# Performance work log

Hardware: AMD Instinct MI355X
Metric: run time of the kernel (lower is better)

## Reference

```python
import jax, jax.numpy as jnp
import numpy as np

B, H, E, R, T = 2048, 512, 300, 512, 50


def setup_inputs() -> dict:
    key = jax.random.key(0)
    ks = jax.random.split(key, 12)
    s = 0.02  # xavier-ish scale for params
    return {
        "x": jax.random.normal(ks[0], (B, E), jnp.float32),
        "h_enc": jax.random.normal(ks[1], (B, R), jnp.float32),
        "phi_history": jax.random.normal(ks[2], (T, B, H), jnp.float32),
        "cell_history": jax.random.normal(ks[3], (T, B, H), jnp.float32),
        "h_summ": jax.random.normal(ks[4], (B, H), jnp.float32),
        "c_summ": jax.random.normal(ks[5], (B, H), jnp.float32),
        "W_w": jax.random.normal(ks[6], (4 * H, H + E), jnp.float32) * s,
        "W_b": jnp.zeros((4 * H,), jnp.float32),
        "v_w": jax.random.normal(ks[7], (1, H), jnp.float32) * s,
        "v_b": jnp.zeros((1,), jnp.float32),
        "lq_w": jax.random.normal(ks[8], (H, R), jnp.float32) * s,
        "lq_b": jnp.zeros((H,), jnp.float32),
        "lk_w": jax.random.normal(ks[9], (H, H), jnp.float32) * s,
        "lk_b": jnp.zeros((H,), jnp.float32),
        "ls_w": jax.random.normal(ks[10], (H, H), jnp.float32) * s,
        "ls_b": jnp.zeros((H,), jnp.float32),
    }


def reference(x, h_enc, phi_history, cell_history, h_summ, c_summ,
              W_w, W_b, v_w, v_b, lq_w, lq_b, lk_w, lk_b, ls_w, ls_b):
    Hd = h_summ.shape[-1]
    # [T,B,H] -> [B,T,H] (torch.stack(...).transpose(0,1))
    phi = jnp.transpose(phi_history, (1, 0, 2))
    cell = jnp.transpose(cell_history, (1, 0, 2))
    # additive attention over cached history
    q = h_enc @ lq_w.T + lq_b                       # [B,H]
    k = jnp.einsum('bth,ah->bta', phi, lk_w) + lk_b  # [B,T,H]
    su = h_summ @ ls_w.T + ls_b                     # [B,H]
    e = jnp.tanh(q[:, None, :] + k + su[:, None, :])
    scores = jnp.einsum('bth,oh->bto', e, v_w)[..., 0] + v_b[0]  # [B,T]
    p = jax.nn.softmax(scores, axis=-1)
    h_s = jnp.einsum('bt,bth->bh', p, phi)
    c_s = jnp.einsum('bt,bth->bh', p, cell)
    # fused LSTM gates on [h_summ, x]
    gates = jnp.concatenate([h_s, x], axis=1) @ W_w.T + W_b  # [B,4H]
    f_t = jax.nn.sigmoid(gates[:, :Hd])
    o_t = jax.nn.sigmoid(gates[:, Hd:2 * Hd])
    i_t = jax.nn.sigmoid(gates[:, 2 * Hd:3 * Hd])
    ch_t = jnp.tanh(gates[:, 3 * Hd:])
    c_ctrl = f_t * c_s + i_t * ch_t
    h_ctrl = o_t * jnp.tanh(c_ctrl)
    return h_ctrl
```

## Files before the change

### kernel.cpp

```cpp
#include <hip/hip_runtime.h>
#include <math.h>

#define Bm 2048
#define Hm 512
#define Em 300
#define Tm 50
#define KWm 812
#define KWp 832

typedef unsigned short u16;
typedef unsigned int u32;
typedef __attribute__((ext_vector_type(8))) short short8;
typedef __attribute__((ext_vector_type(8))) u16 ushort8v;
typedef __attribute__((ext_vector_type(4))) float f32x4;

__device__ __forceinline__ float sigmoidf_(float x) { return 1.f / (1.f + __expf(-x)); }
__device__ __forceinline__ float tanhfast(float x) { return 1.f - 2.f / (__expf(2.f * x) + 1.f); }

__device__ __forceinline__ u16 bfr(float x) {
    union { float f; u32 u; } c; c.f = x;
    u32 u = c.u;
    u += 0x7FFFu + ((u >> 16) & 1u);
    return (u16)(u >> 16);
}
__device__ __forceinline__ ushort8v cvt8(const float* __restrict__ p) {
    f32x4 v0 = *(const f32x4*)p;
    f32x4 v1 = *(const f32x4*)(p + 4);
    ushort8v r;
    r[0] = bfr(v0[0]); r[1] = bfr(v0[1]); r[2] = bfr(v0[2]); r[3] = bfr(v0[3]);
    r[4] = bfr(v1[0]); r[5] = bfr(v1[1]); r[6] = bfr(v1[2]); r[7] = bfr(v1[3]);
    return r;
}

__device__ __forceinline__ void gload16(const u16* g, u16* l) {
    __builtin_amdgcn_global_load_lds((const __attribute__((address_space(1))) void*)g,
                                     (__attribute__((address_space(3))) void*)l, 16, 0, 0);
}

__global__ __launch_bounds__(256) void k_prep(
        const float* __restrict__ henc, const float* __restrict__ hsum,
        const float* __restrict__ lq, const float* __restrict__ ls,
        const float* __restrict__ Ww, const float* __restrict__ x,
        const float* __restrict__ lkw,
        const float* __restrict__ lqb, const float* __restrict__ lsb,
        const float* __restrict__ lkb, const float* __restrict__ phi,
        u16* __restrict__ Wg, u16* __restrict__ Xb, u16* __restrict__ lkwb,
        float* __restrict__ qbias, u16* __restrict__ phib,
        float* __restrict__ qs) {
    const int job = blockIdx.y;
    const int r = blockIdx.x;
    const int tid = threadIdx.x;
    if (job == 0) {
        for (int c = tid; c < KWp; c += 256)
            Wg[(size_t)r * KWp + c] = (c < KWm) ? bfr(Ww[(size_t)r * KWm + c]) : (u16)0;
    } else if (job == 1) {
        for (int c = 512 + tid; c < KWp; c += 256)
            Xb[(size_t)r * KWp + c] = (c < KWm) ? bfr(x[(size_t)r * Em + (c - 512)]) : (u16)0;
        if (r < 512)
            for (int c = tid; c < 512; c += 256)
                lkwb[(size_t)r * 512 + c] = bfr(lkw[(size_t)r * 512 + c]);
        if (r == 0)
            for (int c = tid; c < 512; c += 256)
                qbias[c] = lqb[c] + lsb[c] + lkb[c];
    } else if (job == 2) {
        const size_t nvec = (size_t)Tm * Bm * 512 / 8;
        for (size_t i = (size_t)r * 256 + tid; i < nvec; i += (size_t)2048 * 256)
            *(ushort8v*)&phib[i * 8] = cvt8(phi + i * 8);
    } else {
        if (r >= 512) return;
        __shared__ u16 Asl[64 * 32];
        __shared__ u16 Bsl[64 * 32];
        const int z = r & 1;
        const int n0 = ((r >> 1) & 7) * 64;
        const int m0 = (r >> 4) * 64;
        const float* A = z ? hsum : henc;
        const float* W = z ? ls : lq;
        const int lane = tid & 63, wid = tid >> 6;
        const int wr = wid >> 1, wc = wid & 1;
        const int l15 = lane & 15, l4 = lane >> 4;
        const int srow = tid >> 2;
        const int gch  = tid & 3;
        const int sslot = gch ^ ((srow >> 1) & 3);
        f32x4 acc[2][2];
        #pragma unroll
        for (int i = 0; i < 2; ++i)
            #pragma unroll
            for (int j = 0; j < 2; ++j) acc[i][j] = (f32x4){0.f, 0.f, 0.f, 0.f};
        for (int k0 = 0; k0 < 512; k0 += 32) {
            __syncthreads();
            *(ushort8v*)&Asl[srow * 32 + sslot * 8] =
                cvt8(A + (size_t)(m0 + srow) * 512 + k0 + gch * 8);
            *(ushort8v*)&Bsl[srow * 32 + sslot * 8] =
                cvt8(W + (size_t)(n0 + srow) * 512 + k0 + gch * 8);
            __syncthreads();
            short8 af[2], bf[2];
            #pragma unroll
            for (int mf = 0; mf < 2; ++mf) {
                int rr = wr * 32 + mf * 16 + l15;
                af[mf] = *(const short8*)&Asl[rr * 32 + (l4 ^ ((rr >> 1) & 3)) * 8];
            }
            #pragma unroll
            for (int nf = 0; nf < 2; ++nf) {
                int rr = wc * 32 + nf * 16 + l15;
                bf[nf] = *(const short8*)&Bsl[rr * 32 + (l4 ^ ((rr >> 1) & 3)) * 8];
            }
            #pragma unroll
            for (int mf = 0; mf < 2; ++mf)
                #pragma unroll
                for (int nf = 0; nf < 2; ++nf)
                    acc[mf][nf] = __builtin_amdgcn_mfma_f32_16x16x32_bf16(
                                      af[mf], bf[nf], acc[mf][nf], 0, 0, 0);
        }
        #pragma unroll
        for (int mf = 0; mf < 2; ++mf)
            #pragma unroll
            for (int nf = 0; nf < 2; ++nf)
                #pragma unroll
                for (int reg = 0; reg < 4; ++reg) {
                    int b = m0 + wr * 32 + mf * 16 + l4 * 4 + reg;
                    int h = n0 + wc * 32 + nf * 16 + l15;
                    atomicAdd(&qs[(size_t)b * Hm + h], acc[mf][nf][reg]);
                }
    }
}

__global__ __launch_bounds__(512, 4) void k_scores_mfma(
        const u16* __restrict__ phib, const u16* __restrict__ lkwb,
        const float* __restrict__ qs2, const float* __restrict__ vw,
        const float* __restrict__ qbias, float* __restrict__ scores) {
    __shared__ u16 Asl[256 * 64];
    __shared__ u16 Bsl[128 * 64];
    const int d  = blockIdx.x;
    const int wg = (d & 7) * 200 + (d >> 3);
    const int n0 = (wg & 3) << 7;
    const int m0 = (wg >> 2) << 8;
    const int t  = m0 >> 11;
    const int b0 = m0 & (Bm - 1);
    const int tid = threadIdx.x, lane = tid & 63, wid = tid >> 6;
    const int wm = wid >> 1, wn = wid & 1;
    const int l15 = lane & 15, l4 = lane >> 4;
    const int rin = lane >> 3;
    const int schunk = (lane & 7) ^ rin;

    f32x4 acc[4][4];
    #pragma unroll
    for (int i = 0; i < 4; ++i)
        #pragma unroll
        for (int j = 0; j < 4; ++j) acc[i][j] = (f32x4){0.f, 0.f, 0.f, 0.f};

    for (int kt = 0; kt < 8; ++kt) {
        const int k0 = kt << 6;
        __syncthreads();
        #pragma unroll
        for (int j = 0; j < 4; ++j) {
            int r = (wid << 5) + (j << 3) + rin;
            gload16(phib + (size_t)(m0 + r) * 512 + k0 + schunk * 8,
                    &Asl[((wid << 5) + (j << 3)) * 64]);
        }
        #pragma unroll
        for (int j = 0; j < 2; ++j) {
            int r = (wid << 4) + (j << 3) + rin;
            gload16(lkwb + (size_t)(n0 + r) * 512 + k0 + schunk * 8,
                    &Bsl[((wid << 4) + (j << 3)) * 64]);
        }
        __syncthreads();
        __builtin_amdgcn_s_setprio(1);
        #pragma unroll
        for (int ks = 0; ks < 2; ++ks) {
            short8 af[4], bf[4];
            const int c = ks * 4 + l4;
            #pragma unroll
            for (int mf = 0; mf < 4; ++mf) {
                int r = wm * 64 + mf * 16 + l15;
                af[mf] = *(const short8*)&Asl[r * 64 + (c ^ (r & 7)) * 8];
            }
            #pragma unroll
            for (int nf = 0; nf < 4; ++nf) {
                int r = wn * 64 + nf * 16 + l15;
                bf[nf] = *(const short8*)&Bsl[r * 64 + (c ^ (r & 7)) * 8];
            }
            #pragma unroll
            for (int mf = 0; mf < 4; ++mf)
                #pragma unroll
                for (int nf = 0; nf < 4; ++nf)
                    acc[mf][nf] = __builtin_amdgcn_mfma_f32_16x16x32_bf16(
                                      af[mf], bf[nf], acc[mf][nf], 0, 0, 0);
        }
        __builtin_amdgcn_s_setprio(0);
    }

    float vws[4], qb[4];
    int av[4];
    #pragma unroll
    for (int nf = 0; nf < 4; ++nf) {
        av[nf] = n0 + wn * 64 + nf * 16 + l15;
        vws[nf] = vw[av[nf]];
        qb[nf]  = qbias[av[nf]];
    }
    #pragma unroll
    for (int mf = 0; mf < 4; ++mf) {
        #pragma unroll
        for (int reg = 0; reg < 4; ++reg) {
            int b = b0 + wm * 64 + mf * 16 + l4 * 4 + reg;
            const float* q = qs2 + (size_t)b * Hm;
            float s = 0.f;
            #pragma unroll
            for (int nf = 0; nf < 4; ++nf)
                s = fmaf(tanhfast(acc[mf][nf][reg] + q[av[nf]] + qb[nf]), vws[nf], s);
            #pragma unroll
            for (int o = 1; o < 16; o <<= 1) s += __shfl_xor(s, o);
            if (l15 == 0) atomicAdd(&scores[(size_t)b * Tm + t], s);
        }
    }
}

__global__ __launch_bounds__(256) void k_attn(
        const u16* __restrict__ phib, const float* __restrict__ cell,
        const float* __restrict__ scores,
        u16* __restrict__ Xb, float* __restrict__ cs) {
    __shared__ float p[Tm];
    const int b = blockIdx.x;
    const int tid = threadIdx.x;
    if (tid < 64) {
        float s = (tid < Tm) ? scores[(size_t)b * Tm + tid] : -INFINITY;
        float m = s;
        #pragma unroll
        for (int o = 32; o; o >>= 1) m = fmaxf(m, __shfl_xor(m, o));
        float ex = (tid < Tm) ? __expf(s - m) : 0.f;
        float sum = ex;
        #pragma unroll
        for (int o = 32; o; o >>= 1) sum += __shfl_xor(sum, o);
        if (tid < Tm) p[tid] = ex / sum;
    }
    __syncthreads();
    const int c0 = tid * 2;
    float ah0 = 0.f, ah1 = 0.f, ac0 = 0.f, ac1 = 0.f;
    for (int t = 0; t < Tm; ++t) {
        float w = p[t];
        const size_t rb = ((size_t)t * Bm + b) * 512 + c0;
        u32 ph2 = *(const u32*)&phib[rb];
        float2 ce2 = *(const float2*)&cell[rb];
        float p0 = __uint_as_float(ph2 << 16);
        float p1 = __uint_as_float(ph2 & 0xFFFF0000u);
        ah0 = fmaf(w, p0, ah0);
        ah1 = fmaf(w, p1, ah1);
        ac0 = fmaf(w, ce2.x, ac0);
        ac1 = fmaf(w, ce2.y, ac1);
    }
    *(u32*)&Xb[(size_t)b * KWp + c0] = (u32)bfr(ah0) | ((u32)bfr(ah1) << 16);
    *(float2*)&cs[(size_t)b * Hm + c0] = make_float2(ac0, ac1);
}

__global__ __launch_bounds__(256) void k_gates_mfma(
        const u16* __restrict__ Xb, const u16* __restrict__ Wg,
        float* __restrict__ gates) {
    __shared__ u16 Asl[64 * 64];
    __shared__ u16 Bsl[128 * 64];
    const int d  = blockIdx.x;
    const int wg = (d & 7) * 64 + (d >> 3);
    const int m0 = (wg & 31) << 6;
    const int n0 = (wg >> 5) << 7;
    const int tid = threadIdx.x, lane = tid & 63, wid = tid >> 6;
    const int wr = wid >> 1, wc = wid & 1;
    const int l15 = lane & 15, l4 = lane >> 4;
    const int rin = lane >> 3;
    const int schunk = (lane & 7) ^ rin;
    f32x4 acc[2][4];
    #pragma unroll
    for (int i = 0; i < 2; ++i)
        #pragma unroll
        for (int j = 0; j < 4; ++j) acc[i][j] = (f32x4){0.f, 0.f, 0.f, 0.f};

    for (int kt = 0; kt < 13; ++kt) {
        const int k0 = kt << 6;
        __syncthreads();
        #pragma unroll
        for (int j = 0; j < 2; ++j) {
            int r = (wid << 4) + (j << 3) + rin;
            gload16(Xb + (size_t)(m0 + r) * KWp + k0 + schunk * 8,
                    &Asl[((wid << 4) + (j << 3)) * 64]);
        }
        #pragma unroll
        for (int j = 0; j < 4; ++j) {
            int r = (wid << 5) + (j << 3) + rin;
            gload16(Wg + (size_t)(n0 + r) * KWp + k0 + schunk * 8,
                    &Bsl[((wid << 5) + (j << 3)) * 64]);
        }
        __syncthreads();
        short8 af[2][2], bf[4][2];
        #pragma unroll
        for (int mf = 0; mf < 2; ++mf) {
            int r = wr * 32 + mf * 16 + l15;
            #pragma unroll
            for (int ks = 0; ks < 2; ++ks) {
                int c = ks * 4 + l4;
                af[mf][ks] = *(const short8*)&Asl[r * 64 + (c ^ (r & 7)) * 8];
            }
        }
        #pragma unroll
        for (int nf = 0; nf < 4; ++nf) {
            int r = wc * 64 + nf * 16 + l15;
            #pragma unroll
            for (int ks = 0; ks < 2; ++ks) {
                int c = ks * 4 + l4;
                bf[nf][ks] = *(const short8*)&Bsl[r * 64 + (c ^ (r & 7)) * 8];
            }
        }
        __builtin_amdgcn_s_setprio(1);
        #pragma unroll
        for (int ks = 0; ks < 2; ++ks)
            #pragma unroll
            for (int mf = 0; mf < 2; ++mf)
                #pragma unroll
                for (int nf = 0; nf < 4; ++nf)
                    acc[mf][nf] = __builtin_amdgcn_mfma_f32_16x16x32_bf16(
                                      af[mf][ks], bf[nf][ks], acc[mf][nf], 0, 0, 0);
        __builtin_amdgcn_s_setprio(0);
    }
    #pragma unroll
    for (int mf = 0; mf < 2; ++mf)
        #pragma unroll
        for (int nf = 0; nf < 4; ++nf)
            #pragma unroll
            for (int reg = 0; reg < 4; ++reg) {
                int b = m0 + wr * 32 + mf * 16 + l4 * 4 + reg;
                int n = n0 + wc * 64 + nf * 16 + l15;
                gates[(size_t)b * 2048 + n] = acc[mf][nf][reg];
            }
}

__global__ __launch_bounds__(256) void k_lstm(
        const float* __restrict__ gates, const float* __restrict__ Wb,
        const float* __restrict__ cs, float* __restrict__ out) {
    const int idx = blockIdx.x * 256 + threadIdx.x;
    const int b = idx >> 9, h = idx & 511;
    const float* g = gates + (size_t)b * 2048;
    float f  = sigmoidf_(g[h]        + Wb[h]);
    float o  = sigmoidf_(g[512 + h]  + Wb[512 + h]);
    float ii = sigmoidf_(g[1024 + h] + Wb[1024 + h]);
    float ch = tanhfast( g[1536 + h] + Wb[1536 + h]);
    float c  = f * cs[idx] + ii * ch;
    out[idx] = o * tanhfast(c);
}

extern "C" void kernel_launch(void* const* d_in, const int* in_sizes, int n_in,
                              void* d_out, int out_size, void* d_ws, size_t ws_size,
                              hipStream_t stream) {
    const float* x      = (const float*)d_in[0];
    const float* h_enc  = (const float*)d_in[1];
    const float* phi    = (const float*)d_in[2];
    const float* cell   = (const float*)d_in[3];
    const float* h_summ = (const float*)d_in[4];
    const float* W_w    = (const float*)d_in[6];
    const float* W_b    = (const float*)d_in[7];
    const float* v_w    = (const float*)d_in[8];
    const float* lq_w   = (const float*)d_in[10];
    const float* lq_b   = (const float*)d_in[11];
    const float* lk_w   = (const float*)d_in[12];
    const float* lk_b   = (const float*)d_in[13];
    const float* ls_w   = (const float*)d_in[14];
    const float* ls_b   = (const float*)d_in[15];
    float* out = (float*)d_out;

    char* w = (char*)d_ws;
    u16*   phib   = (u16*)  (w);
    float* gates  = (float*)(w);
    float* qs     = (float*)(w + 104857600);
    float* scores = (float*)(w + 109051904);
    float* cs     = (float*)(w + 109461504);
    u16*   Wg     = (u16*)  (w + 113655808);
    u16*   Xb     = (u16*)  (w + 117063680);
    u16*   lkwb   = (u16*)  (w + 120471552);
    float* qbias  = (float*)(w + 121520128);

    hipMemsetAsync(qs, 0, 4194304 + (size_t)Bm * Tm * sizeof(float), stream);
    k_prep<<<dim3(2048, 4), 256, 0, stream>>>(h_enc, h_summ, lq_w, ls_w, W_w, x, lk_w,
                                              lq_b, ls_b, lk_b, phi,
                                              Wg, Xb, lkwb, qbias, phib, qs);
    k_scores_mfma<<<dim3(1600), 512, 0, stream>>>(phib, lkwb, qs, v_w, qbias, scores);
    k_attn<<<dim3(Bm), 256, 0, stream>>>(phib, cell, scores, Xb, cs);
    k_gates_mfma<<<dim3(512), 256, 0, stream>>>(Xb, Wg, gates);
    k_lstm<<<dim3((Bm * Hm) / 256), 256, 0, stream>>>(gates, W_b, cs, out);
}
```

Before: 273.9 us.

## Double-buffer LDS tiles in scores MFMA kernel with smaller K step

Splits the LDS A/B tiles into two buffers of half the K depth (32 instead of 64) and prefetches the next K slice with direct global-to-LDS loads while MFMAs run on the current one. This removes one barrier per iteration and is meant to hide global load latency behind compute. The swizzle changes to suit 32-element rows. The cost is twice as many loop iterations and barriers, and LDS use stays the same.

```diff
diff --git a/kernel.cpp b/kernel.cpp
--- a/kernel.cpp
+++ b/kernel.cpp
@@ -128,8 +128,8 @@
         const u16* __restrict__ phib, const u16* __restrict__ lkwb,
         const float* __restrict__ qs2, const float* __restrict__ vw,
         const float* __restrict__ qbias, float* __restrict__ scores) {
-    __shared__ u16 Asl[256 * 64];
-    __shared__ u16 Bsl[128 * 64];
+    __shared__ u16 Asl[2][256 * 32];
+    __shared__ u16 Bsl[2][128 * 32];
     const int d  = blockIdx.x;
     const int wg = (d & 7) * 200 + (d >> 3);
     const int n0 = (wg & 3) << 7;
@@ -139,8 +139,8 @@
     const int tid = threadIdx.x, lane = tid & 63, wid = tid >> 6;
     const int wm = wid >> 1, wn = wid & 1;
     const int l15 = lane & 15, l4 = lane >> 4;
-    const int rin = lane >> 3;
-    const int schunk = (lane & 7) ^ rin;
+    const int srw = lane >> 2;
+    const int sch = lane & 3;
 
     f32x4 acc[4][4];
     #pragma unroll
@@ -148,45 +148,50 @@
         #pragma unroll
         for (int j = 0; j < 4; ++j) acc[i][j] = (f32x4){0.f, 0.f, 0.f, 0.f};
 
-    for (int kt = 0; kt < 8; ++kt) {
-        const int k0 = kt << 6;
+    auto STAGE = [&](int buf, int kt) {
+        const int k0 = kt << 5;
+        #pragma unroll
+        for (int j = 0; j < 2; ++j) {
+            int r = (wid << 5) + (j << 4) + srw;
+            int gc = sch ^ ((r >> 1) & 3);
+            gload16(phib + (size_t)(m0 + r) * 512 + k0 + gc * 8,
+                    &Asl[buf][((wid << 5) + (j << 4)) * 32]);
+        }
+        {
+            int r = (wid << 4) + srw;
+            int gc = sch ^ ((r >> 1) & 3);
+            gload16(lkwb + (size_t)(n0 + r) * 512 + k0 + gc * 8,
+                    &Bsl[buf][(wid << 4) * 32]);
+        }
+    };
+
+    STAGE(0, 0);
+    __syncthreads();
+    int cur = 0;
+    #pragma unroll 1
+    for (int kt = 0; kt < 16; ++kt) {
+        if (kt < 15) STAGE(cur ^ 1, kt + 1);
+        short8 af[4], bf[4];
+        #pragma unroll
+        for (int mf = 0; mf < 4; ++mf) {
+            int r = wm * 64 + mf * 16 + l15;
+            af[mf] = *(const short8*)&Asl[cur][r * 32 + (l4 ^ ((r >> 1) & 3)) * 8];
+        }
+        #pragma unroll
+        for (int nf = 0; nf < 4; ++nf) {
+            int r = wn * 64 + nf * 16 + l15;
+            bf[nf] = *(const short8*)&Bsl[cur][r * 32 + (l4 ^ ((r >> 1) & 3)) * 8];
+        }
+        __builtin_amdgcn_s_setprio(1);
+        #pragma unroll
+        for (int mf = 0; mf < 4; ++mf)
+            #pragma unroll
+            for (int nf = 0; nf < 4; ++nf)
+                acc[mf][nf] = __builtin_amdgcn_mfma_f32_16x16x32_bf16(
+                                  af[mf], bf[nf], acc[mf][nf], 0, 0, 0);
+        __builtin_amdgcn_s_setprio(0);
         __syncthreads();
-        #pragma unroll
-        for (int j = 0; j < 4; ++j) {
-            int r = (wid << 5) + (j << 3) + rin;
-            gload16(phib + (size_t)(m0 + r) * 512 + k0 + schunk * 8,
-                    &Asl[((wid << 5) + (j << 3)) * 64]);
-        }
-        #pragma unroll
-        for (int j = 0; j < 2; ++j) {
-            int r = (wid << 4) + (j << 3) + rin;
-            gload16(lkwb + (size_t)(n0 + r) * 512 + k0 + schunk * 8,
-                    &Bsl[((wid << 4) + (j << 3)) * 64]);
-        }
-        __syncthreads();
-        __builtin_amdgcn_s_setprio(1);
-        #pragma unroll
-        for (int ks = 0; ks < 2; ++ks) {
-            short8 af[4], bf[4];
-            const int c = ks * 4 + l4;
-            #pragma unroll
-            for (int mf = 0; mf < 4; ++mf) {
-                int r = wm * 64 + mf * 16 + l15;
-                af[mf] = *(const short8*)&Asl[r * 64 + (c ^ (r & 7)) * 8];
-            }
-            #pragma unroll
-            for (int nf = 0; nf < 4; ++nf) {
-                int r = wn * 64 + nf * 16 + l15;
-                bf[nf] = *(const short8*)&Bsl[r * 64 + (c ^ (r & 7)) * 8];
-            }
-            #pragma unroll
-            for (int mf = 0; mf < 4; ++mf)
-                #pragma unroll
-                for (int nf = 0; nf < 4; ++nf)
-                    acc[mf][nf] = __builtin_amdgcn_mfma_f32_16x16x32_bf16(
-                                      af[mf], bf[nf], acc[mf][nf], 0, 0, 0);
-        }
-        __builtin_amdgcn_s_setprio(0);
+        cur ^= 1;
     }
 
     float vws[4], qb[4];
```

New measurement: 281.2 us. 1.03x slower.

## Interleave gate weight rows and fuse LSTM epilogue into gates GEMM

Applied to the files above, without the earlier changes.

Weight rows are permuted during prep so the four gates (f,o,i,c~) for each hidden unit land in adjacent output columns. The gates GEMM epilogue then adds the bias, gathers the four gate values with lane shuffles, and computes the LSTM cell output directly. This removes the separate k_lstm launch and the write and re-read of the 16 MB gates buffer. In exchange only a quarter of lanes do the output math, and the stores are strided per hidden unit.

```diff
diff --git a/kernel.cpp b/kernel.cpp
--- a/kernel.cpp
+++ b/kernel.cpp
@@ -51,8 +51,10 @@
     const int r = blockIdx.x;
     const int tid = threadIdx.x;
     if (job == 0) {
+        const int h = r >> 2, g = r & 3;
+        const float* src = Ww + (size_t)(g * 512 + h) * KWm;
         for (int c = tid; c < KWp; c += 256)
-            Wg[(size_t)r * KWp + c] = (c < KWm) ? bfr(Ww[(size_t)r * KWm + c]) : (u16)0;
+            Wg[(size_t)r * KWp + c] = (c < KWm) ? bfr(src[c]) : (u16)0;
     } else if (job == 1) {
         for (int c = 512 + tid; c < KWp; c += 256)
             Xb[(size_t)r * KWp + c] = (c < KWm) ? bfr(x[(size_t)r * Em + (c - 512)]) : (u16)0;
@@ -253,7 +255,8 @@
 
 __global__ __launch_bounds__(256) void k_gates_mfma(
         const u16* __restrict__ Xb, const u16* __restrict__ Wg,
-        float* __restrict__ gates) {
+        const float* __restrict__ Wb, const float* __restrict__ cs,
+        float* __restrict__ out) {
     __shared__ u16 Asl[64 * 64];
     __shared__ u16 Bsl[128 * 64];
     const int d  = blockIdx.x;
@@ -317,30 +320,33 @@
                                       af[mf][ks], bf[nf][ks], acc[mf][nf], 0, 0, 0);
         __builtin_amdgcn_s_setprio(0);
     }
-    #pragma unroll
-    for (int mf = 0; mf < 2; ++mf)
-        #pragma unroll
-        for (int nf = 0; nf < 4; ++nf)
+
+    const int g = l15 & 3;
+    #pragma unroll
+    for (int mf = 0; mf < 2; ++mf) {
+        #pragma unroll
+        for (int nf = 0; nf < 4; ++nf) {
+            int col = n0 + wc * 64 + nf * 16 + l15;
+            int h = col >> 2;
+            float wb = Wb[g * 512 + h];
             #pragma unroll
             for (int reg = 0; reg < 4; ++reg) {
                 int b = m0 + wr * 32 + mf * 16 + l4 * 4 + reg;
-                int n = n0 + wc * 64 + nf * 16 + l15;
-                gates[(size_t)b * 2048 + n] = acc[mf][nf][reg];
-            }
-}
-
-__global__ __launch_bounds__(256) void k_lstm(
-        const float* __restrict__ gates, const float* __restrict__ Wb,
-        const float* __restrict__ cs, float* __restrict__ out) {
-    const int idx = blockIdx.x * 256 + threadIdx.x;
-    const int b = idx >> 9, h = idx & 511;
-    const float* g = gates + (size_t)b * 2048;
-    float f  = sigmoidf_(g[h]        + Wb[h]);
-    float o  = sigmoidf_(g[512 + h]  + Wb[512 + h]);
-    float ii = sigmoidf_(g[1024 + h] + Wb[1024 + h]);
-    float ch = tanhfast( g[1536 + h] + Wb[1536 + h]);
-    float c  = f * cs[idx] + ii * ch;
-    out[idx] = o * tanhfast(c);
+                float v = acc[mf][nf][reg] + wb;
+                float a1 = __shfl_xor(v, 1);
+                float a2 = __shfl_xor(v, 2);
+                float a3 = __shfl_xor(a1, 2);
+                if (g == 0) {
+                    float f  = sigmoidf_(v);
+                    float o  = sigmoidf_(a1);
+                    float ii = sigmoidf_(a2);
+                    float ch = tanhfast(a3);
+                    float c  = f * cs[(size_t)b * Hm + h] + ii * ch;
+                    out[(size_t)b * Hm + h] = o * tanhfast(c);
+                }
+            }
+        }
+    }
 }
 
 extern "C" void kernel_launch(void* const* d_in, const int* in_sizes, int n_in,
@@ -364,7 +370,6 @@
 
     char* w = (char*)d_ws;
     u16*   phib   = (u16*)  (w);
-    float* gates  = (float*)(w);
     float* qs     = (float*)(w + 104857600);
     float* scores = (float*)(w + 109051904);
     float* cs     = (float*)(w + 109461504);
@@ -379,6 +384,5 @@
                                               Wg, Xb, lkwb, qbias, phib, qs);
     k_scores_mfma<<<dim3(1600), 512, 0, stream>>>(phib, lkwb, qs, v_w, qbias, scores);
     k_attn<<<dim3(Bm), 256, 0, stream>>>(phib, cell, scores, Xb, cs);
-    k_gates_mfma<<<dim3(512), 256, 0, stream>>>(Xb, Wg, gates);
-    k_lstm<<<dim3((Bm * Hm) / 256), 256, 0, stream>>>(gates, W_b, cs, out);
-}
+    k_gates_mfma<<<dim3(512), 256, 0, stream>>>(Xb, Wg, W_b, cs, out);
+}
```

Measured after the change: 282.9 us. 1.03x slower.
